# Kernel optimization log

Hardware: AMD Instinct MI355X
Metric: run time of the kernel (lower is better)

## Reference

```python
import jax, jax.numpy as jnp
import numpy as np

N_NODES = 100000
N_EDGES = 1600000


def _degree_norms(src, dst, n):
    ones = jnp.ones((src.shape[0],), dtype=jnp.float32)
    out_deg = jax.ops.segment_sum(ones, src, num_segments=n)
    in_deg = jax.ops.segment_sum(ones, dst, num_segments=n)
    norm_src = jax.lax.rsqrt(jnp.clip(out_deg, 1.0))  # D_src^{-1/2}
    norm_dst = jax.lax.rsqrt(jnp.clip(in_deg, 1.0))   # D_dst^{-1/2}
    return norm_src, norm_dst


def _graph_conv(x, W, b, src, dst, norm_src, norm_dst):
    # DGL GraphConv, norm='both': h = D_dst^{-1/2} A (D_src^{-1/2} x W) + b
    h = (x * norm_src[:, None]) @ W              # [N, out] dense transform
    agg = jax.ops.segment_sum(h[src], dst, num_segments=x.shape[0])  # SpMM
    return agg * norm_dst[:, None] + b


def setup_inputs() -> dict:
    key = jax.random.key(0)
    ks = jax.random.split(key, 8)
    in_feat = jax.random.normal(ks[0], (N_NODES, 128), dtype=jnp.float32)
    src = jax.random.randint(ks[1], (N_EDGES,), 0, N_NODES, dtype=jnp.int64)
    dst = jax.random.randint(ks[2], (N_EDGES,), 0, N_NODES, dtype=jnp.int64)
    def glorot(k, fan_in, fan_out):
        s = jnp.sqrt(6.0 / (fan_in + fan_out)).astype(jnp.float32)
        return jax.random.uniform(k, (fan_in, fan_out), jnp.float32, -s, s)
    W1 = glorot(ks[3], 128, 128); b1 = jnp.zeros((128,), jnp.float32)
    W2 = glorot(ks[4], 128, 128); b2 = jnp.zeros((128,), jnp.float32)
    W3 = glorot(ks[5], 128, 128); b3 = jnp.zeros((128,), jnp.float32)
    W4 = glorot(ks[6], 128, 64);  b4 = jnp.zeros((64,), jnp.float32)
    return {"in_feat": in_feat, "src": src, "dst": dst,
            "W1": W1, "b1": b1, "W2": W2, "b2": b2,
            "W3": W3, "b3": b3, "W4": W4, "b4": b4}


def reference(in_feat, src, dst, W1, b1, W2, b2, W3, b3, W4, b4):
    norm_src, norm_dst = _degree_norms(src, dst, in_feat.shape[0])
    h = jax.nn.relu(_graph_conv(in_feat, W1, b1, src, dst, norm_src, norm_dst))
    h = jax.nn.relu(_graph_conv(h, W2, b2, src, dst, norm_src, norm_dst))
    h = jax.nn.relu(_graph_conv(h, W3, b3, src, dst, norm_src, norm_dst))
    h = _graph_conv(h, W4, b4, src, dst, norm_src, norm_dst)
    return h
```

## Files before the change

### kernel.cpp

```cpp
#include <hip/hip_runtime.h>

#define N_NODES 100000
#define N_EDGES 1600000
#define CAP 60

typedef _Float16 half8 __attribute__((ext_vector_type(8)));
typedef float f32x4 __attribute__((ext_vector_type(4)));

__device__ __forceinline__ bool idx_is64(const int* flag) { return *flag == 0; }
__device__ __forceinline__ int load_idx(const void* p, int e, bool is64) {
  return is64 ? (int)((const long long*)p)[e] : ((const int*)p)[e];
}

__global__ void detect_k(const unsigned* __restrict__ w, int* __restrict__ flag,
                         int* __restrict__ cs, int* __restrict__ cnt) {
  int tid = blockIdx.x * 256 + threadIdx.x;
  for (int i = tid; i < N_NODES; i += 65536) { cs[i] = 0; cnt[i] = 0; }
  if (blockIdx.x == 0) {
    unsigned acc = 0;
    for (int i = threadIdx.x; i < 2048; i += 256) acc |= w[2 * i + 1];
    unsigned long long m = __ballot(acc != 0);
    if ((threadIdx.x & 63) == 0 && m != 0ULL) atomicOr(flag, 1);
  }
}

__global__ void build_k(const void* __restrict__ src, const void* __restrict__ dst,
                        const int* __restrict__ flag, int* __restrict__ cs,
                        int* __restrict__ cnt, int* __restrict__ bucket) {
  int e = blockIdx.x * 256 + threadIdx.x;
  if (e >= N_EDGES) return;
  bool is64 = idx_is64(flag);
  int s = load_idx(src, e, is64);
  int d = load_idx(dst, e, is64);
  atomicAdd(&cs[s], 1);
  int pos = atomicAdd(&cnt[d], 1);
  if (pos < CAP) bucket[d * CAP + pos] = s;
}

__global__ void norm_k(int* __restrict__ cs_ns, const int* __restrict__ cnt,
                       float* __restrict__ nd) {
  int i = blockIdx.x * blockDim.x + threadIdx.x;
  if (i >= N_NODES) return;
  int a = cs_ns[i];
  ((float*)cs_ns)[i] = rsqrtf((float)(a > 1 ? a : 1));
  int b = cnt[i];
  nd[i] = rsqrtf((float)(b > 1 ? b : 1));
}

template <int OUT>
__global__ __launch_bounds__(512) void mgemm_k(const float* __restrict__ X,
                                               const float* __restrict__ W,
                                               float* __restrict__ H) {
  constexpr int NT = OUT / 16;
  constexpr int WS = 136;
  __shared__ _Float16 Wh[OUT * WS];
  __shared__ _Float16 Wl[OUT * WS];
  const int t = threadIdx.x;
  for (int i = t; i < 128 * OUT; i += 512) {
    int k = i / OUT, c = i % OUT;
    float w = W[i];
    _Float16 hi = (_Float16)w;
    Wh[c * WS + k] = hi;
    Wl[c * WS + k] = (_Float16)(w - (float)hi);
  }
  __syncthreads();

  const int wave = t >> 6, lane = t & 63;
  const int tb = blockIdx.x * 256 + wave * 32;
  const int frow = lane & 15;
  const int kb = (lane >> 4) * 8;

  f32x4 acc[2][NT];
#pragma unroll
  for (int rg = 0; rg < 2; rg++)
#pragma unroll
    for (int ct = 0; ct < NT; ct++) acc[rg][ct] = (f32x4){0.f, 0.f, 0.f, 0.f};

#pragma unroll
  for (int ks = 0; ks < 4; ks++) {
    half8 Ah[2], Al[2];
#pragma unroll
    for (int rg = 0; rg < 2; rg++) {
      int r = tb + rg * 16 + frow;
      float4 x0 = make_float4(0.f, 0.f, 0.f, 0.f), x1 = x0;
      if (r < N_NODES) {
        const float* Xr = X + (size_t)r * 128 + ks * 32 + kb;
        x0 = *(const float4*)Xr;
        x1 = *(const float4*)(Xr + 4);
      }
      float xf[8] = {x0.x, x0.y, x0.z, x0.w, x1.x, x1.y, x1.z, x1.w};
      half8 h, l;
#pragma unroll
      for (int j = 0; j < 8; j++) {
        _Float16 hi = (_Float16)xf[j];
        h[j] = hi;
        l[j] = (_Float16)(xf[j] - (float)hi);
      }
      Ah[rg] = h;
      Al[rg] = l;
    }
#pragma unroll
    for (int ct = 0; ct < NT; ct++) {
      const int wo = (ct * 16 + frow) * WS + ks * 32 + kb;
      half8 Bh = *(const half8*)&Wh[wo];
      half8 Bl = *(const half8*)&Wl[wo];
#pragma unroll
      for (int rg = 0; rg < 2; rg++) {
        acc[rg][ct] = __builtin_amdgcn_mfma_f32_16x16x32_f16(Ah[rg], Bh, acc[rg][ct], 0, 0, 0);
        acc[rg][ct] = __builtin_amdgcn_mfma_f32_16x16x32_f16(Al[rg], Bh, acc[rg][ct], 0, 0, 0);
        acc[rg][ct] = __builtin_amdgcn_mfma_f32_16x16x32_f16(Ah[rg], Bl, acc[rg][ct], 0, 0, 0);
      }
    }
  }

  const int dr = (lane >> 4) * 4, dc = lane & 15;
#pragma unroll
  for (int rg = 0; rg < 2; rg++) {
#pragma unroll
    for (int j = 0; j < 4; j++) {
      int r = tb + rg * 16 + dr + j;
      if (r < N_NODES) {
#pragma unroll
        for (int ct = 0; ct < NT; ct++)
          H[(size_t)r * OUT + ct * 16 + dc] = acc[rg][ct][j];
      }
    }
  }
}

template <bool SCALE_SRC>
__global__ __launch_bounds__(256) void agg_k(
    const float* __restrict__ h, const int* __restrict__ cnt,
    const int* __restrict__ bucket, const float* __restrict__ ns,
    const float* __restrict__ nd, const float* __restrict__ bprev,
    float* __restrict__ Xout) {
  const int t = threadIdx.x;
  const int wave = t >> 6, lane = t & 63;
  const int j = lane >> 5, q = lane & 31;
  const int n = blockIdx.x * 4 + wave;
  if (n >= N_NODES) return;
  int m = cnt[n];
  m = m < CAP ? m : CAP;
  const int* bk = bucket + n * CAP;
  float4 acc = make_float4(0.f, 0.f, 0.f, 0.f);
  for (int e = j; e < m; e += 2) {
    int s = bk[e];
    float4 v = *(const float4*)&h[(size_t)s * 128 + q * 4];
    if constexpr (SCALE_SRC) {
      float w = ns[s];
      acc.x += v.x * w; acc.y += v.y * w; acc.z += v.z * w; acc.w += v.w * w;
    } else {
      acc.x += v.x; acc.y += v.y; acc.z += v.z; acc.w += v.w;
    }
  }
  acc.x += __shfl_xor(acc.x, 32);
  acc.y += __shfl_xor(acc.y, 32);
  acc.z += __shfl_xor(acc.z, 32);
  acc.w += __shfl_xor(acc.w, 32);
  if (j == 0) {
    float sd = nd[n], sc = ns[n];
    float4 bp = *(const float4*)&bprev[q * 4];
    float4 o;
    o.x = fmaxf(acc.x * sd + bp.x, 0.f) * sc;
    o.y = fmaxf(acc.y * sd + bp.y, 0.f) * sc;
    o.z = fmaxf(acc.z * sd + bp.z, 0.f) * sc;
    o.w = fmaxf(acc.w * sd + bp.w, 0.f) * sc;
    *(float4*)&Xout[(size_t)n * 128 + q * 4] = o;
  }
}

__global__ __launch_bounds__(256) void final_k(
    const float* __restrict__ h4, const int* __restrict__ cnt,
    const int* __restrict__ bucket, const float* __restrict__ nd,
    const float* __restrict__ b4, float* __restrict__ outp) {
  const int t = threadIdx.x;
  const int wave = t >> 6, lane = t & 63;
  const int j = lane >> 4, q = lane & 15;
  const int n = blockIdx.x * 4 + wave;
  if (n >= N_NODES) return;
  int m = cnt[n];
  m = m < CAP ? m : CAP;
  const int* bk = bucket + n * CAP;
  float4 acc = make_float4(0.f, 0.f, 0.f, 0.f);
  for (int e = j; e < m; e += 4) {
    int s = bk[e];
    float4 v = *(const float4*)&h4[(size_t)s * 64 + q * 4];
    acc.x += v.x; acc.y += v.y; acc.z += v.z; acc.w += v.w;
  }
  acc.x += __shfl_xor(acc.x, 16);
  acc.y += __shfl_xor(acc.y, 16);
  acc.z += __shfl_xor(acc.z, 16);
  acc.w += __shfl_xor(acc.w, 16);
  acc.x += __shfl_xor(acc.x, 32);
  acc.y += __shfl_xor(acc.y, 32);
  acc.z += __shfl_xor(acc.z, 32);
  acc.w += __shfl_xor(acc.w, 32);
  if (j == 0) {
    float sd = nd[n];
    float4 bb = *(const float4*)&b4[q * 4];
    float4 o = make_float4(acc.x * sd + bb.x, acc.y * sd + bb.y,
                           acc.z * sd + bb.z, acc.w * sd + bb.w);
    *(float4*)&outp[(size_t)n * 64 + q * 4] = o;
  }
}

extern "C" void kernel_launch(void* const* d_in, const int* in_sizes, int n_in,
                              void* d_out, int out_size, void* d_ws, size_t ws_size,
                              hipStream_t stream) {
  const float* in_feat = (const float*)d_in[0];
  const void* src = d_in[1];
  const void* dst = d_in[2];
  const float* W1 = (const float*)d_in[3];
  const float* b1 = (const float*)d_in[4];
  const float* W2 = (const float*)d_in[5];
  const float* b2 = (const float*)d_in[6];
  const float* W3 = (const float*)d_in[7];
  const float* b3 = (const float*)d_in[8];
  const float* W4 = (const float*)d_in[9];
  const float* b4 = (const float*)d_in[10];

  char* ws = (char*)d_ws;
  float* hA = (float*)(ws + 0);
  float* hB = (float*)(ws + 51200000);
  float* ns = (float*)(ws + 102400000);
  float* nd = (float*)(ws + 102800000);
  int* flag = (int*)(ws + 103200000);

  const size_t WS_NEED = 103200064ull + 24000000ull + 400000ull;
  const bool ws_fits = ws_size >= WS_NEED;
  int* bucket = ws_fits ? (int*)(ws + 103200064) : (int*)d_out;
  int* cnt = ws_fits ? (int*)(ws + 127200064) : (int*)((char*)d_out + 24000000);

  hipMemsetAsync(flag, 0, 4, stream);
  detect_k<<<256, 256, 0, stream>>>((const unsigned*)src, flag, (int*)ns, cnt);
  build_k<<<(N_EDGES + 255) / 256, 256, 0, stream>>>(src, dst, flag, (int*)ns, cnt, bucket);
  norm_k<<<(N_NODES + 255) / 256, 256, 0, stream>>>((int*)ns, cnt, nd);

  const int GB = (N_NODES + 255) / 256;
  const int AB = (N_NODES + 3) / 4;
  mgemm_k<128><<<GB, 512, 0, stream>>>(in_feat, W1, hA);
  agg_k<true><<<AB, 256, 0, stream>>>(hA, cnt, bucket, ns, nd, b1, hB);
  mgemm_k<128><<<GB, 512, 0, stream>>>(hB, W2, hA);
  agg_k<false><<<AB, 256, 0, stream>>>(hA, cnt, bucket, ns, nd, b2, hB);
  mgemm_k<128><<<GB, 512, 0, stream>>>(hB, W3, hA);
  agg_k<false><<<AB, 256, 0, stream>>>(hA, cnt, bucket, ns, nd, b3, hB);
  mgemm_k<64><<<GB, 512, 0, stream>>>(hB, W4, hA);
  if (ws_fits) {
    final_k<<<AB, 256, 0, stream>>>(hA, cnt, bucket, nd, b4, (float*)d_out);
  } else {
    final_k<<<AB, 256, 0, stream>>>(hA, cnt, bucket, nd, b4, hB);
    hipMemcpyAsync(d_out, hB, (size_t)N_NODES * 64 * 4, hipMemcpyDeviceToDevice, stream);
  }
}
```

Measured before the change: 670.6 us.

## Fuse graph build into first GEMM and compute dst norm inline

```diff
diff --git a/kernel.cpp b/kernel.cpp
--- a/kernel.cpp
+++ b/kernel.cpp
@@ -3,48 +3,119 @@
 #define N_NODES 100000
 #define N_EDGES 1600000
 #define CAP 60
+#define GB 391
+#define EPB ((N_EDGES + GB - 1) / GB)
 
 typedef _Float16 half8 __attribute__((ext_vector_type(8)));
 typedef float f32x4 __attribute__((ext_vector_type(4)));
 
-__device__ __forceinline__ bool idx_is64(const int* flag) { return *flag == 0; }
-__device__ __forceinline__ int load_idx(const void* p, int e, bool is64) {
+__device__ __forceinline__ int load_idx(const void* p, long long e, bool is64) {
   return is64 ? (int)((const long long*)p)[e] : ((const int*)p)[e];
 }
 
-__global__ void detect_k(const unsigned* __restrict__ w, int* __restrict__ flag,
-                         int* __restrict__ cs, int* __restrict__ cnt) {
-  int tid = blockIdx.x * 256 + threadIdx.x;
-  for (int i = tid; i < N_NODES; i += 65536) { cs[i] = 0; cnt[i] = 0; }
-  if (blockIdx.x == 0) {
-    unsigned acc = 0;
-    for (int i = threadIdx.x; i < 2048; i += 256) acc |= w[2 * i + 1];
-    unsigned long long m = __ballot(acc != 0);
-    if ((threadIdx.x & 63) == 0 && m != 0ULL) atomicOr(flag, 1);
-  }
-}
-
-__global__ void build_k(const void* __restrict__ src, const void* __restrict__ dst,
-                        const int* __restrict__ flag, int* __restrict__ cs,
-                        int* __restrict__ cnt, int* __restrict__ bucket) {
-  int e = blockIdx.x * 256 + threadIdx.x;
-  if (e >= N_EDGES) return;
-  bool is64 = idx_is64(flag);
-  int s = load_idx(src, e, is64);
-  int d = load_idx(dst, e, is64);
-  atomicAdd(&cs[s], 1);
-  int pos = atomicAdd(&cnt[d], 1);
-  if (pos < CAP) bucket[d * CAP + pos] = s;
-}
-
-__global__ void norm_k(int* __restrict__ cs_ns, const int* __restrict__ cnt,
-                       float* __restrict__ nd) {
+__global__ void norm_k(int* __restrict__ cs_ns) {
   int i = blockIdx.x * blockDim.x + threadIdx.x;
   if (i >= N_NODES) return;
   int a = cs_ns[i];
   ((float*)cs_ns)[i] = rsqrtf((float)(a > 1 ? a : 1));
-  int b = cnt[i];
-  nd[i] = rsqrtf((float)(b > 1 ? b : 1));
+}
+
+template <int OUT>
+__global__ __launch_bounds__(512) void build_mgemm_k(
+    const float* __restrict__ X, const float* __restrict__ W, float* __restrict__ H,
+    const void* __restrict__ src, const void* __restrict__ dst,
+    int* __restrict__ cs, int* __restrict__ cnt, int* __restrict__ bucket) {
+  const int t = threadIdx.x;
+  const int wave = t >> 6, lane = t & 63;
+
+  unsigned accw = 0;
+  for (int i = lane; i < 2048; i += 64) accw |= ((const unsigned*)src)[2 * i + 1];
+  const bool is64 = (__ballot(accw != 0) == 0ULL);
+  const long long e0 = (long long)blockIdx.x * EPB;
+  for (int i = t; i < EPB; i += 512) {
+    long long e = e0 + i;
+    if (e < N_EDGES) {
+      int s = load_idx(src, e, is64);
+      int d = load_idx(dst, e, is64);
+      atomicAdd(&cs[s], 1);
+      int pos = atomicAdd(&cnt[d], 1);
+      if (pos < CAP) bucket[d * CAP + pos] = s;
+    }
+  }
+
+  constexpr int NT = OUT / 16;
+  constexpr int WS = 136;
+  __shared__ _Float16 Wh[OUT * WS];
+  __shared__ _Float16 Wl[OUT * WS];
+  for (int i = t; i < 128 * OUT; i += 512) {
+    int k = i / OUT, c = i % OUT;
+    float w = W[i];
+    _Float16 hi = (_Float16)w;
+    Wh[c * WS + k] = hi;
+    Wl[c * WS + k] = (_Float16)(w - (float)hi);
+  }
+  __syncthreads();
+
+  const int tb = blockIdx.x * 256 + wave * 32;
+  const int frow = lane & 15;
+  const int kb = (lane >> 4) * 8;
+
+  f32x4 acc[2][NT];
+#pragma unroll
+  for (int rg = 0; rg < 2; rg++)
+#pragma unroll
+    for (int ct = 0; ct < NT; ct++) acc[rg][ct] = (f32x4){0.f, 0.f, 0.f, 0.f};
+
+#pragma unroll
+  for (int ks = 0; ks < 4; ks++) {
+    half8 Ah[2], Al[2];
+#pragma unroll
+    for (int rg = 0; rg < 2; rg++) {
+      int r = tb + rg * 16 + frow;
+      float4 x0 = make_float4(0.f, 0.f, 0.f, 0.f), x1 = x0;
+      if (r < N_NODES) {
+        const float* Xr = X + (size_t)r * 128 + ks * 32 + kb;
+        x0 = *(const float4*)Xr;
+        x1 = *(const float4*)(Xr + 4);
+      }
+      float xf[8] = {x0.x, x0.y, x0.z, x0.w, x1.x, x1.y, x1.z, x1.w};
+      half8 h, l;
+#pragma unroll
+      for (int j = 0; j < 8; j++) {
+        _Float16 hi = (_Float16)xf[j];
+        h[j] = hi;
+        l[j] = (_Float16)(xf[j] - (float)hi);
+      }
+      Ah[rg] = h;
+      Al[rg] = l;
+    }
+#pragma unroll
+    for (int ct = 0; ct < NT; ct++) {
+      const int wo = (ct * 16 + frow) * WS + ks * 32 + kb;
+      half8 Bh = *(const half8*)&Wh[wo];
+      half8 Bl = *(const half8*)&Wl[wo];
+#pragma unroll
+      for (int rg = 0; rg < 2; rg++) {
+        acc[rg][ct] = __builtin_amdgcn_mfma_f32_16x16x32_f16(Ah[rg], Bh, acc[rg][ct], 0, 0, 0);
+        acc[rg][ct] = __builtin_amdgcn_mfma_f32_16x16x32_f16(Al[rg], Bh, acc[rg][ct], 0, 0, 0);
+        acc[rg][ct] = __builtin_amdgcn_mfma_f32_16x16x32_f16(Ah[rg], Bl, acc[rg][ct], 0, 0, 0);
+      }
+    }
+  }
+
+  const int dr = (lane >> 4) * 4, dc = lane & 15;
+#pragma unroll
+  for (int rg = 0; rg < 2; rg++) {
+#pragma unroll
+    for (int j = 0; j < 4; j++) {
+      int r = tb + rg * 16 + dr + j;
+      if (r < N_NODES) {
+#pragma unroll
+        for (int ct = 0; ct < NT; ct++)
+          H[(size_t)r * OUT + ct * 16 + dc] = acc[rg][ct][j];
+      }
+    }
+  }
 }
 
 template <int OUT>
@@ -132,15 +203,14 @@
 __global__ __launch_bounds__(256) void agg_k(
     const float* __restrict__ h, const int* __restrict__ cnt,
     const int* __restrict__ bucket, const float* __restrict__ ns,
-    const float* __restrict__ nd, const float* __restrict__ bprev,
-    float* __restrict__ Xout) {
+    const float* __restrict__ bprev, float* __restrict__ Xout) {
   const int t = threadIdx.x;
   const int wave = t >> 6, lane = t & 63;
   const int j = lane >> 5, q = lane & 31;
   const int n = blockIdx.x * 4 + wave;
   if (n >= N_NODES) return;
-  int m = cnt[n];
-  m = m < CAP ? m : CAP;
+  int mr = cnt[n];
+  int m = mr < CAP ? mr : CAP;
   const int* bk = bucket + n * CAP;
   float4 acc = make_float4(0.f, 0.f, 0.f, 0.f);
   for (int e = j; e < m; e += 2) {
@@ -158,7 +228,8 @@
   acc.z += __shfl_xor(acc.z, 32);
   acc.w += __shfl_xor(acc.w, 32);
   if (j == 0) {
-    float sd = nd[n], sc = ns[n];
+    float sd = rsqrtf((float)(mr > 1 ? mr : 1));
+    float sc = ns[n];
     float4 bp = *(const float4*)&bprev[q * 4];
     float4 o;
     o.x = fmaxf(acc.x * sd + bp.x, 0.f) * sc;
@@ -171,15 +242,15 @@
 
 __global__ __launch_bounds__(256) void final_k(
     const float* __restrict__ h4, const int* __restrict__ cnt,
-    const int* __restrict__ bucket, const float* __restrict__ nd,
-    const float* __restrict__ b4, float* __restrict__ outp) {
+    const int* __restrict__ bucket, const float* __restrict__ b4,
+    float* __restrict__ outp) {
   const int t = threadIdx.x;
   const int wave = t >> 6, lane = t & 63;
   const int j = lane >> 4, q = lane & 15;
   const int n = blockIdx.x * 4 + wave;
   if (n >= N_NODES) return;
-  int m = cnt[n];
-  m = m < CAP ? m : CAP;
+  int mr = cnt[n];
+  int m = mr < CAP ? mr : CAP;
   const int* bk = bucket + n * CAP;
   float4 acc = make_float4(0.f, 0.f, 0.f, 0.f);
   for (int e = j; e < m; e += 4) {
@@ -196,7 +267,7 @@
   acc.z += __shfl_xor(acc.z, 32);
   acc.w += __shfl_xor(acc.w, 32);
   if (j == 0) {
-    float sd = nd[n];
+    float sd = rsqrtf((float)(mr > 1 ? mr : 1));
     float4 bb = *(const float4*)&b4[q * 4];
     float4 o = make_float4(acc.x * sd + bb.x, acc.y * sd + bb.y,
                            acc.z * sd + bb.z, acc.w * sd + bb.w);
@@ -223,32 +294,29 @@
   float* hA = (float*)(ws + 0);
   float* hB = (float*)(ws + 51200000);
   float* ns = (float*)(ws + 102400000);
-  float* nd = (float*)(ws + 102800000);
-  int* flag = (int*)(ws + 103200000);
-
-  const size_t WS_NEED = 103200064ull + 24000000ull + 400000ull;
+  int* cnt = (int*)(ws + 102800000);
+
+  const size_t WS_NEED = 103200000ull + 24000000ull;
   const bool ws_fits = ws_size >= WS_NEED;
-  int* bucket = ws_fits ? (int*)(ws + 103200064) : (int*)d_out;
-  int* cnt = ws_fits ? (int*)(ws + 127200064) : (int*)((char*)d_out + 24000000);
-
-  hipMemsetAsync(flag, 0, 4, stream);
-  detect_k<<<256, 256, 0, stream>>>((const unsigned*)src, flag, (int*)ns, cnt);
-  build_k<<<(N_EDGES + 255) / 256, 256, 0, stream>>>(src, dst, flag, (int*)ns, cnt, bucket);
-  norm_k<<<(N_NODES + 255) / 256, 256, 0, stream>>>((int*)ns, cnt, nd);
-
-  const int GB = (N_NODES + 255) / 256;
+  int* bucket = ws_fits ? (int*)(ws + 103200000) : (int*)d_out;
+
+  hipMemsetAsync(ns, 0, 800000, stream);
+
+  build_mgemm_k<128><<<GB, 512, 0, stream>>>(in_feat, W1, hA, src, dst,
+                                             (int*)ns, cnt, bucket);
+  norm_k<<<(N_NODES + 255) / 256, 256, 0, stream>>>((int*)ns);
+
   const int AB = (N_NODES + 3) / 4;
-  mgemm_k<128><<<GB, 512, 0, stream>>>(in_feat, W1, hA);
-  agg_k<true><<<AB, 256, 0, stream>>>(hA, cnt, bucket, ns, nd, b1, hB);
+  agg_k<true><<<AB, 256, 0, stream>>>(hA, cnt, bucket, ns, b1, hB);
   mgemm_k<128><<<GB, 512, 0, stream>>>(hB, W2, hA);
-  agg_k<false><<<AB, 256, 0, stream>>>(hA, cnt, bucket, ns, nd, b2, hB);
+  agg_k<false><<<AB, 256, 0, stream>>>(hA, cnt, bucket, ns, b2, hB);
   mgemm_k<128><<<GB, 512, 0, stream>>>(hB, W3, hA);
-  agg_k<false><<<AB, 256, 0, stream>>>(hA, cnt, bucket, ns, nd, b3, hB);
+  agg_k<false><<<AB, 256, 0, stream>>>(hA, cnt, bucket, ns, b3, hB);
   mgemm_k<64><<<GB, 512, 0, stream>>>(hB, W4, hA);
   if (ws_fits) {
-    final_k<<<AB, 256, 0, stream>>>(hA, cnt, bucket, nd, b4, (float*)d_out);
+    final_k<<<AB, 256, 0, stream>>>(hA, cnt, bucket, b4, (float*)d_out);
   } else {
-    final_k<<<AB, 256, 0, stream>>>(hA, cnt, bucket, nd, b4, hB);
+    final_k<<<AB, 256, 0, stream>>>(hA, cnt, bucket, b4, hB);
     hipMemcpyAsync(d_out, hB, (size_t)N_NODES * 64 * 4, hipMemcpyDeviceToDevice, stream);
   }
 }
```

After: 656.8 us. -2.1%, faster.
